# Kernel optimization log

Hardware: AMD Instinct MI355X
Metric: run time of the kernel (lower is better)

Reference implementation:

```python
import jax, jax.numpy as jnp
import numpy as np

B, N, E, DIN, H1, H2, DOUT = 2, 20000, 320000, 128, 256, 256, 128


def setup_inputs() -> dict:
    key = jax.random.key(0)
    ks = jax.random.split(key, 9)
    X = jax.random.normal(ks[0], (B, N, DIN), dtype=jnp.float32)
    edge_index = jax.random.randint(ks[1], (2, E), 0, N, dtype=jnp.int32)
    def lin(k, fan_in, fan_out):
        lim = 1.0 / np.sqrt(fan_in)
        return jax.random.uniform(k, (fan_in, fan_out), jnp.float32, -lim, lim)
    W1 = lin(ks[2], DIN, H1); b1 = jnp.zeros((H1,), jnp.float32)
    W2 = lin(ks[3], H1, H2);  b2 = jnp.zeros((H2,), jnp.float32)
    W3 = lin(ks[4], H2, DOUT); b3 = jnp.zeros((DOUT,), jnp.float32)
    prelu_a = jnp.array(0.25, jnp.float32)  # PReLU default single shared param
    return dict(X=X, W1=W1, b1=b1, W2=W2, b2=b2, W3=W3, b3=b3,
                prelu_a=prelu_a, edge_index=edge_index)


def reference(X, W1, b1, W2, b2, W3, b3, prelu_a, edge_index):
    src, dst = edge_index[0], edge_index[1]
    n = X.shape[1]
    # GCN symmetric normalization with self-loops: deg = in-degree + 1
    deg = jax.ops.segment_sum(jnp.ones_like(src, X.dtype), dst, num_segments=n) + 1.0
    dinv = jax.lax.rsqrt(deg)                      # [N]
    norm_e = dinv[src] * dinv[dst]                 # [E] edge norm
    norm_self = dinv * dinv                        # [N] self-loop norm

    def gcn(x, W, b):
        h = x @ W                                  # [N, F_out]
        agg = jax.ops.segment_sum(h[src] * norm_e[:, None], dst, num_segments=n)
        agg = agg + h * norm_self[:, None]         # add self-loop message
        return agg + b

    def prelu(x):
        return jnp.where(x >= 0, x, prelu_a * x)

    def single(x):  # x: [N, DIN]
        x = prelu(gcn(x, W1, b1))
        x = prelu(gcn(x, W2, b2))
        return gcn(x, W3, b3)

    return jax.vmap(single)(X)                     # [B, N, DOUT]
```

## Files before the change

### kernel.cpp

```cpp
#include <hip/hip_runtime.h>

#define NB 20000
#define EB 320000
#define DIN 128
#define H1D 256
#define H2D 256
#define DOUTD 128
#define SCAN_BLOCKS ((NB + 255) / 256)


__global__ void zero_kernel(int* __restrict__ p, int n) {
    int t = blockIdx.x * blockDim.x + threadIdx.x;
    if (t < n) p[t] = 0;
}

__global__ void hist_kernel(const int* __restrict__ dst, int* __restrict__ bins) {
    int t = blockIdx.x * blockDim.x + threadIdx.x;
    if (t < EB) atomicAdd(&bins[dst[t]], 1);
}

__global__ __launch_bounds__(256) void scanA_kernel(const int* __restrict__ bins,
                                                    int* __restrict__ loc,
                                                    int* __restrict__ blksum) {
    __shared__ int s[256];
    int t = threadIdx.x;
    int i = blockIdx.x * 256 + t;
    int v = (i < NB) ? bins[i] : 0;
    s[t] = v;
    __syncthreads();
    for (int off = 1; off < 256; off <<= 1) {
        int u = (t >= off) ? s[t - off] : 0;
        __syncthreads();
        s[t] += u;
        __syncthreads();
    }
    if (i < NB) loc[i] = s[t] - v;
    if (t == 255) blksum[blockIdx.x] = s[255];
}

__global__ __launch_bounds__(128) void scanB_kernel(int* __restrict__ blksum) {
    __shared__ int s[128];
    int t = threadIdx.x;
    int v = (t < SCAN_BLOCKS) ? blksum[t] : 0;
    s[t] = v;
    __syncthreads();
    for (int off = 1; off < 128; off <<= 1) {
        int u = (t >= off) ? s[t - off] : 0;
        __syncthreads();
        s[t] += u;
        __syncthreads();
    }
    if (t < SCAN_BLOCKS) blksum[t] = s[t] - v;
}

__global__ __launch_bounds__(256) void scanC_kernel(const int* __restrict__ bins,
                                                    const int* __restrict__ loc,
                                                    const int* __restrict__ blksum,
                                                    int* __restrict__ rs,
                                                    int* __restrict__ cursor,
                                                    float* __restrict__ dinv) {
    int i = blockIdx.x * 256 + threadIdx.x;
    if (i < NB) {
        int r = loc[i] + blksum[blockIdx.x];
        rs[i] = r;
        cursor[i] = r;
        dinv[i] = rsqrtf((float)bins[i] + 1.0f);
    }
    if (i == 0) rs[NB] = EB;
}

__global__ void scatter_kernel(const int* __restrict__ src, const int* __restrict__ dst,
                               const float* __restrict__ dinv,
                               int* __restrict__ cursor, int2* __restrict__ edges) {
    int t = blockIdx.x * blockDim.x + threadIdx.x;
    if (t < EB) {
        int d = dst[t], s = src[t];
        int p = atomicAdd(&cursor[d], 1);
        edges[p] = make_int2(s, __float_as_int(dinv[s] * dinv[d]));
    }
}


__device__ inline void vload(float (&d)[4], const float* p) {
    float4 t = *(const float4*)p; d[0] = t.x; d[1] = t.y; d[2] = t.z; d[3] = t.w;
}
__device__ inline void vload(float (&d)[2], const float* p) {
    float2 t = *(const float2*)p; d[0] = t.x; d[1] = t.y;
}
__device__ inline void vstore(float* p, const float (&d)[4]) {
    *(float4*)p = make_float4(d[0], d[1], d[2], d[3]);
}
__device__ inline void vstore(float* p, const float (&d)[2]) {
    *(float2*)p = make_float2(d[0], d[1]);
}

template <int F, bool BIAS, bool PRELU>
__device__ void agg_body(int ablk,
                         const float* __restrict__ h, float* __restrict__ out,
                         const int* __restrict__ rs, const int2* __restrict__ edges,
                         const float* __restrict__ dinv, const float* __restrict__ bias,
                         const float* __restrict__ pa) {
    constexpr int VEC = F / 64;
    int wid = threadIdx.x >> 6;
    int lane = threadIdx.x & 63;
    int node = ablk * 4 + wid;
    const float* hsrc = h + (size_t)lane * VEC;

    float acc0[VEC], acc1[VEC] = {}, acc2[VEC] = {}, acc3[VEC] = {};
    {
        float dv = dinv[node];
        float sw = dv * dv;
        float t[VEC];
        vload(t, hsrc + (size_t)node * F);
#pragma unroll
        for (int v = 0; v < VEC; ++v) acc0[v] = t[v] * sw;
    }
    int e0 = __builtin_amdgcn_readfirstlane(rs[node]);
    int e1 = __builtin_amdgcn_readfirstlane(rs[node + 1]);
    int e = e0;
    for (; e + 4 <= e1; e += 4) {
        int2 d0 = edges[e], d1 = edges[e + 1], d2 = edges[e + 2], d3 = edges[e + 3];
        float t0[VEC], t1[VEC], t2[VEC], t3[VEC];
        vload(t0, hsrc + (size_t)d0.x * F);
        vload(t1, hsrc + (size_t)d1.x * F);
        vload(t2, hsrc + (size_t)d2.x * F);
        vload(t3, hsrc + (size_t)d3.x * F);
        float w0 = __int_as_float(d0.y), w1 = __int_as_float(d1.y);
        float w2 = __int_as_float(d2.y), w3 = __int_as_float(d3.y);
#pragma unroll
        for (int v = 0; v < VEC; ++v) {
            acc0[v] = fmaf(t0[v], w0, acc0[v]);
            acc1[v] = fmaf(t1[v], w1, acc1[v]);
            acc2[v] = fmaf(t2[v], w2, acc2[v]);
            acc3[v] = fmaf(t3[v], w3, acc3[v]);
        }
    }
    for (; e < e1; ++e) {
        int2 d0 = edges[e];
        float t0[VEC];
        vload(t0, hsrc + (size_t)d0.x * F);
        float w0 = __int_as_float(d0.y);
#pragma unroll
        for (int v = 0; v < VEC; ++v) acc0[v] = fmaf(t0[v], w0, acc0[v]);
    }
#pragma unroll
    for (int v = 0; v < VEC; ++v) acc0[v] += (acc1[v] + acc2[v]) + acc3[v];
    if (BIAS) {
        float bv[VEC];
        vload(bv, bias + lane * VEC);
#pragma unroll
        for (int v = 0; v < VEC; ++v) acc0[v] += bv[v];
    }
    if (PRELU) {
        float a = *pa;
#pragma unroll
        for (int v = 0; v < VEC; ++v) acc0[v] = acc0[v] >= 0.0f ? acc0[v] : a * acc0[v];
    }
    vstore(out + (size_t)node * F + lane * VEC, acc0);
}

template <bool BIAS, bool PRELU>
__device__ void gemm_body(int gx, const float* __restrict__ A, int M, int K,
                          const float* __restrict__ W, int Nc,
                          const float* __restrict__ bias, const float* __restrict__ pa,
                          float* __restrict__ C, int mt) {
    __shared__ alignas(16) float As[16][132];
    __shared__ alignas(16) float Bs[16][68];
    int t = threadIdx.x;
    int bm = (gx % mt) * 128;
    int bn = (gx / mt) * 64;
    int tx = t & 15, ty = t >> 4;
    int m0 = ty * 8, n0 = tx * 4;
    int ar = t >> 2, ac4 = (t & 3) * 4;
    int br = t >> 4, bc4 = (t & 15) * 4;

    float acc[8][4] = {};

    for (int k0 = 0; k0 < K; k0 += 16) {
        float4 a0 = make_float4(0.f, 0.f, 0.f, 0.f), a1 = a0;
        int r0 = bm + ar, r1 = bm + ar + 64;
        if (r0 < M) a0 = *(const float4*)&A[(size_t)r0 * K + k0 + ac4];
        if (r1 < M) a1 = *(const float4*)&A[(size_t)r1 * K + k0 + ac4];
        As[ac4 + 0][ar] = a0.x; As[ac4 + 1][ar] = a0.y;
        As[ac4 + 2][ar] = a0.z; As[ac4 + 3][ar] = a0.w;
        As[ac4 + 0][ar + 64] = a1.x; As[ac4 + 1][ar + 64] = a1.y;
        As[ac4 + 2][ar + 64] = a1.z; As[ac4 + 3][ar + 64] = a1.w;
        float4 bv = *(const float4*)&W[(size_t)(k0 + br) * Nc + bn + bc4];
        *(float4*)&Bs[br][bc4] = bv;
        __syncthreads();
#pragma unroll
        for (int k = 0; k < 16; ++k) {
            float4 av0 = *(const float4*)&As[k][m0];
            float4 av1 = *(const float4*)&As[k][m0 + 4];
            float4 bv4 = *(const float4*)&Bs[k][n0];
            float a_[8] = {av0.x, av0.y, av0.z, av0.w, av1.x, av1.y, av1.z, av1.w};
            float b_[4] = {bv4.x, bv4.y, bv4.z, bv4.w};
#pragma unroll
            for (int i = 0; i < 8; ++i)
#pragma unroll
                for (int j = 0; j < 4; ++j)
                    acc[i][j] = fmaf(a_[i], b_[j], acc[i][j]);
        }
        __syncthreads();
    }

    float pav = 0.0f;
    if (PRELU) pav = *pa;
#pragma unroll
    for (int i = 0; i < 8; ++i) {
        int row = bm + m0 + i;
        if (row < M) {
            float v[4];
#pragma unroll
            for (int j = 0; j < 4; ++j) {
                float x = acc[i][j];
                if (BIAS) x += bias[bn + n0 + j];
                if (PRELU) x = (x >= 0.0f) ? x : pav * x;
                v[j] = x;
            }
            *(float4*)&C[(size_t)row * Nc + bn + n0] = make_float4(v[0], v[1], v[2], v[3]);
        }
    }
}


template <int F, bool BIAS, bool PRELU>
__global__ __launch_bounds__(256) void agg_kernel(
    const float* __restrict__ h, float* __restrict__ out,
    const int* __restrict__ rs, const int2* __restrict__ edges,
    const float* __restrict__ dinv, const float* __restrict__ bias,
    const float* __restrict__ pa) {
    agg_body<F, BIAS, PRELU>(blockIdx.x, h, out, rs, edges, dinv, bias, pa);
}

template <bool BIAS, bool PRELU>
__global__ __launch_bounds__(256) void gemm_kernel(
    const float* __restrict__ A, int M, int K, const float* __restrict__ W, int Nc,
    const float* __restrict__ bias, const float* __restrict__ pa,
    float* __restrict__ C, int mt) {
    gemm_body<BIAS, PRELU>(blockIdx.x, A, M, K, W, Nc, bias, pa, C, mt);
}

template <int AF, bool AB, bool AP, bool GB, bool GP>
__global__ __launch_bounds__(256) void fat_kernel(
    const float* __restrict__ A, int M, int K, const float* __restrict__ W, int Nc,
    const float* __restrict__ gbias, float* __restrict__ C, int mt, int ng,
    const float* __restrict__ ah, float* __restrict__ aout,
    const int* __restrict__ rs, const int2* __restrict__ edges,
    const float* __restrict__ dinv, const float* __restrict__ abias,
    const float* __restrict__ pa, int total) {
    int bx = blockIdx.x;
    int p0 = (int)((long long)bx * ng / total);
    int p1 = (int)(((long long)bx + 1) * ng / total);
    if (p1 > p0) {
        gemm_body<GB, GP>(p0, A, M, K, W, Nc, gbias, pa, C, mt);
    } else {
        agg_body<AF, AB, AP>(bx - p1, ah, aout, rs, edges, dinv, abias, pa);
    }
}


static inline char* carve(char*& p, size_t bytes) {
    char* r = p;
    p += (bytes + 255) & ~(size_t)255;
    return r;
}

extern "C" void kernel_launch(void* const* d_in, const int* in_sizes, int n_in,
                              void* d_out, int out_size, void* d_ws, size_t ws_size,
                              hipStream_t stream) {
    const float* X  = (const float*)d_in[0];
    const float* W1 = (const float*)d_in[1];
    const float* b1 = (const float*)d_in[2];
    const float* W2 = (const float*)d_in[3];
    const float* b2 = (const float*)d_in[4];
    const float* W3 = (const float*)d_in[5];
    const float* b3 = (const float*)d_in[6];
    const float* pa = (const float*)d_in[7];
    const int* ei   = (const int*)d_in[8];
    const int* src = ei;
    const int* dst = ei + EB;
    float* out = (float*)d_out;

    char* p = (char*)d_ws;
    int* bins    = (int*)carve(p, NB * sizeof(int));
    int* loc     = (int*)carve(p, NB * sizeof(int));
    int* blksum  = (int*)carve(p, 128 * sizeof(int));
    int* rs      = (int*)carve(p, (NB + 1) * sizeof(int));
    int* cursor  = (int*)carve(p, NB * sizeof(int));
    int2* edges  = (int2*)carve(p, EB * sizeof(int2));
    float* dinv  = (float*)carve(p, NB * sizeof(float));
    float* P0 = (float*)carve(p, (size_t)NB * 256 * sizeof(float));
    float* Q0 = (float*)carve(p, (size_t)NB * 256 * sizeof(float));
    float* P1 = (float*)carve(p, (size_t)NB * 256 * sizeof(float));
    float* Q1 = (float*)carve(p, (size_t)NB * 256 * sizeof(float));

    const float* X0 = X;
    const float* X1 = X + (size_t)NB * DIN;
    float* out0 = out;
    float* out1 = out + (size_t)NB * DOUTD;

    zero_kernel<<<SCAN_BLOCKS, 256, 0, stream>>>(bins, NB);
    hist_kernel<<<(EB + 255) / 256, 256, 0, stream>>>(dst, bins);
    scanA_kernel<<<SCAN_BLOCKS, 256, 0, stream>>>(bins, loc, blksum);
    scanB_kernel<<<1, 128, 0, stream>>>(blksum);
    scanC_kernel<<<SCAN_BLOCKS, 256, 0, stream>>>(bins, loc, blksum, rs, cursor, dinv);
    scatter_kernel<<<(EB + 255) / 256, 256, 0, stream>>>(src, dst, dinv, cursor, edges);

    const int AGG_BLK = NB / 4;
    const int MT = (NB + 127) / 128;
    const int NG_256 = MT * (256 / 64);
    const int NG_128 = MT * (128 / 64);


    agg_kernel<128, false, false><<<AGG_BLK, 256, 0, stream>>>(
        X0, P0, rs, edges, dinv, nullptr, nullptr);

    fat_kernel<128, false, false, true, true><<<NG_256 + AGG_BLK, 256, 0, stream>>>(
        P0, NB, DIN, W1, H1D, b1, Q0, MT, NG_256,
        X1, P1, rs, edges, dinv, nullptr, pa, NG_256 + AGG_BLK);

    gemm_kernel<false, false><<<NG_256, 256, 0, stream>>>(
        Q0, NB, H1D, W2, H2D, nullptr, nullptr, P0, MT);
    gemm_kernel<true, true><<<NG_256, 256, 0, stream>>>(
        P1, NB, DIN, W1, H1D, b1, pa, Q1, MT);

    fat_kernel<256, true, true, false, false><<<NG_256 + AGG_BLK, 256, 0, stream>>>(
        Q1, NB, H1D, W2, H2D, nullptr, P1, MT, NG_256,
        P0, Q0, rs, edges, dinv, b2, pa, NG_256 + AGG_BLK);

    fat_kernel<256, true, true, false, false><<<NG_128 + AGG_BLK, 256, 0, stream>>>(
        Q0, NB, H2D, W3, DOUTD, nullptr, P0, MT, NG_128,
        P1, Q1, rs, edges, dinv, b2, pa, NG_128 + AGG_BLK);

    fat_kernel<128, true, false, false, false><<<NG_128 + AGG_BLK, 256, 0, stream>>>(
        Q1, NB, H2D, W3, DOUTD, nullptr, P1, MT, NG_128,
        P0, out0, rs, edges, dinv, b3, nullptr, NG_128 + AGG_BLK);

    agg_kernel<128, true, false><<<AGG_BLK, 256, 0, stream>>>(
        P1, out1, rs, edges, dinv, b3, nullptr);
}
```

Before: 444.9 us.

## Slice aggregation by feature columns per XCD, enlarge GEMM tile, add nontemporal accesses

After: 1.081 ms. 2.43x slower.

```diff
diff --git a/kernel.cpp b/kernel.cpp
--- a/kernel.cpp
+++ b/kernel.cpp
@@ -7,6 +7,17 @@
 #define H2D 256
 #define DOUTD 128
 #define SCAN_BLOCKS ((NB + 255) / 256)
+
+typedef __attribute__((ext_vector_type(4))) float fvec4;
+
+__device__ inline float4 ntload4(const float* p) {
+    fvec4 v = __builtin_nontemporal_load((const fvec4*)p);
+    return make_float4(v.x, v.y, v.z, v.w);
+}
+__device__ inline void ntstore4(float* p, float4 v) {
+    fvec4 t; t.x = v.x; t.y = v.y; t.z = v.z; t.w = v.w;
+    __builtin_nontemporal_store(t, (fvec4*)p);
+}
 
 
 __global__ void zero_kernel(int* __restrict__ p, int n) {
@@ -81,82 +92,87 @@
 }
 
 
-__device__ inline void vload(float (&d)[4], const float* p) {
-    float4 t = *(const float4*)p; d[0] = t.x; d[1] = t.y; d[2] = t.z; d[3] = t.w;
-}
-__device__ inline void vload(float (&d)[2], const float* p) {
-    float2 t = *(const float2*)p; d[0] = t.x; d[1] = t.y;
-}
-__device__ inline void vstore(float* p, const float (&d)[4]) {
-    *(float4*)p = make_float4(d[0], d[1], d[2], d[3]);
-}
-__device__ inline void vstore(float* p, const float (&d)[2]) {
-    *(float2*)p = make_float2(d[0], d[1]);
-}
-
-template <int F, bool BIAS, bool PRELU>
-__device__ void agg_body(int ablk,
-                         const float* __restrict__ h, float* __restrict__ out,
-                         const int* __restrict__ rs, const int2* __restrict__ edges,
-                         const float* __restrict__ dinv, const float* __restrict__ bias,
-                         const float* __restrict__ pa) {
-    constexpr int VEC = F / 64;
-    int wid = threadIdx.x >> 6;
-    int lane = threadIdx.x & 63;
-    int node = ablk * 4 + wid;
-    const float* hsrc = h + (size_t)lane * VEC;
-
-    float acc0[VEC], acc1[VEC] = {}, acc2[VEC] = {}, acc3[VEC] = {};
-    {
-        float dv = dinv[node];
-        float sw = dv * dv;
-        float t[VEC];
-        vload(t, hsrc + (size_t)node * F);
-#pragma unroll
-        for (int v = 0; v < VEC; ++v) acc0[v] = t[v] * sw;
-    }
-    int e0 = __builtin_amdgcn_readfirstlane(rs[node]);
-    int e1 = __builtin_amdgcn_readfirstlane(rs[node + 1]);
-    int e = e0;
-    for (; e + 4 <= e1; e += 4) {
-        int2 d0 = edges[e], d1 = edges[e + 1], d2 = edges[e + 2], d3 = edges[e + 3];
-        float t0[VEC], t1[VEC], t2[VEC], t3[VEC];
-        vload(t0, hsrc + (size_t)d0.x * F);
-        vload(t1, hsrc + (size_t)d1.x * F);
-        vload(t2, hsrc + (size_t)d2.x * F);
-        vload(t3, hsrc + (size_t)d3.x * F);
-        float w0 = __int_as_float(d0.y), w1 = __int_as_float(d1.y);
-        float w2 = __int_as_float(d2.y), w3 = __int_as_float(d3.y);
-#pragma unroll
-        for (int v = 0; v < VEC; ++v) {
-            acc0[v] = fmaf(t0[v], w0, acc0[v]);
-            acc1[v] = fmaf(t1[v], w1, acc1[v]);
-            acc2[v] = fmaf(t2[v], w2, acc2[v]);
-            acc3[v] = fmaf(t3[v], w3, acc3[v]);
-        }
-    }
-    for (; e < e1; ++e) {
-        int2 d0 = edges[e];
-        float t0[VEC];
-        vload(t0, hsrc + (size_t)d0.x * F);
-        float w0 = __int_as_float(d0.y);
-#pragma unroll
-        for (int v = 0; v < VEC; ++v) acc0[v] = fmaf(t0[v], w0, acc0[v]);
-    }
-#pragma unroll
-    for (int v = 0; v < VEC; ++v) acc0[v] += (acc1[v] + acc2[v]) + acc3[v];
-    if (BIAS) {
-        float bv[VEC];
-        vload(bv, bias + lane * VEC);
-#pragma unroll
-        for (int v = 0; v < VEC; ++v) acc0[v] += bv[v];
-    }
-    if (PRELU) {
-        float a = *pa;
-#pragma unroll
-        for (int v = 0; v < VEC; ++v) acc0[v] = acc0[v] >= 0.0f ? acc0[v] : a * acc0[v];
-    }
-    vstore(out + (size_t)node * F + lane * VEC, acc0);
+template <int F, bool BIAS, bool PRELU, bool NTE>
+__device__ void aggs_body(int a, int xcd,
+                          const float* __restrict__ h, float* __restrict__ out,
+                          const int* __restrict__ rs, const int2* __restrict__ edges,
+                          const float* __restrict__ dinv, const float* __restrict__ bias,
+                          const float* __restrict__ pa) {
+    constexpr int NS = F / 32;
+    constexpr int NH = 8 / NS;
+    constexpr int CG = (F == 128) ? 125 : 250;
+    constexpr int NPB = NB / NH / CG;
+    constexpr int NPW = NPB / 4;
+
+    const int s32 = xcd & (NS - 1);
+    const int half = xcd / NS;
+    const int chunk = a >> 3;
+    const int wid = threadIdx.x >> 6;
+    const int lane = threadIdx.x & 63;
+    const int li = lane & 31;
+    const int eh = lane >> 5;
+
+    const float* gb = h + s32 * 32 + li;
+    const float pav = PRELU ? *pa : 0.0f;
+    const float bval = BIAS ? bias[s32 * 32 + li] : 0.0f;
+
+    int n = half * (NB / NH) + chunk * NPB + wid * NPW;
+    int e1 = __builtin_amdgcn_readfirstlane(rs[n]);
+    for (int j = 0; j < NPW; ++j, ++n) {
+        int e0 = e1;
+        e1 = __builtin_amdgcn_readfirstlane(rs[n + 1]);
+        float a0 = 0.f, a1 = 0.f, a2 = 0.f, a3 = 0.f;
+        int e = e0;
+        for (; e + 8 <= e1; e += 8) {
+            int s0, s1, s2, s3;
+            float w0, w1, w2, w3;
+            if (NTE) {
+                long long r0 = __builtin_nontemporal_load((const long long*)(edges + e + eh));
+                long long r1 = __builtin_nontemporal_load((const long long*)(edges + e + 2 + eh));
+                long long r2 = __builtin_nontemporal_load((const long long*)(edges + e + 4 + eh));
+                long long r3 = __builtin_nontemporal_load((const long long*)(edges + e + 6 + eh));
+                s0 = (int)r0; w0 = __int_as_float((int)(r0 >> 32));
+                s1 = (int)r1; w1 = __int_as_float((int)(r1 >> 32));
+                s2 = (int)r2; w2 = __int_as_float((int)(r2 >> 32));
+                s3 = (int)r3; w3 = __int_as_float((int)(r3 >> 32));
+            } else {
+                int2 r0 = edges[e + eh], r1 = edges[e + 2 + eh];
+                int2 r2 = edges[e + 4 + eh], r3 = edges[e + 6 + eh];
+                s0 = r0.x; w0 = __int_as_float(r0.y);
+                s1 = r1.x; w1 = __int_as_float(r1.y);
+                s2 = r2.x; w2 = __int_as_float(r2.y);
+                s3 = r3.x; w3 = __int_as_float(r3.y);
+            }
+            float t0 = gb[(size_t)s0 * F];
+            float t1 = gb[(size_t)s1 * F];
+            float t2 = gb[(size_t)s2 * F];
+            float t3 = gb[(size_t)s3 * F];
+            a0 = fmaf(t0, w0, a0);
+            a1 = fmaf(t1, w1, a1);
+            a2 = fmaf(t2, w2, a2);
+            a3 = fmaf(t3, w3, a3);
+        }
+        for (; e + 2 <= e1; e += 2) {
+            int2 r0 = edges[e + eh];
+            a0 = fmaf(gb[(size_t)r0.x * F], __int_as_float(r0.y), a0);
+        }
+        if (e < e1) {
+            int my = e + eh;
+            bool valid = (my < e1);
+            int2 r0 = edges[valid ? my : e];
+            float w = valid ? __int_as_float(r0.y) : 0.0f;
+            a0 = fmaf(gb[(size_t)r0.x * F], w, a0);
+        }
+        float acc = (a0 + a1) + (a2 + a3);
+        acc += __shfl_xor(acc, 32, 64);
+        float dv = dinv[n];
+        float ts = gb[(size_t)n * F];
+        float r = fmaf(ts, dv * dv, acc);
+        if (BIAS) r += bval;
+        if (PRELU) r = (r >= 0.0f) ? r : pav * r;
+        if (eh == 0)
+            __builtin_nontemporal_store(r, out + (size_t)n * F + s32 * 32 + li);
+    }
 }
 
 template <bool BIAS, bool PRELU>
@@ -165,38 +181,43 @@
                           const float* __restrict__ bias, const float* __restrict__ pa,
                           float* __restrict__ C, int mt) {
     __shared__ alignas(16) float As[16][132];
-    __shared__ alignas(16) float Bs[16][68];
+    __shared__ alignas(16) float Bs[16][132];
     int t = threadIdx.x;
     int bm = (gx % mt) * 128;
-    int bn = (gx / mt) * 64;
-    int tx = t & 15, ty = t >> 4;
-    int m0 = ty * 8, n0 = tx * 4;
+    int bn = (gx / mt) * 128;
+    int tx = t & 31, ty = t >> 5;
+    int m0 = ty * 16, n0 = tx * 4;
     int ar = t >> 2, ac4 = (t & 3) * 4;
-    int br = t >> 4, bc4 = (t & 15) * 4;
-
-    float acc[8][4] = {};
+    int bk = t >> 4, bc4 = (t & 15) * 4;
+
+    float acc[16][4] = {};
 
     for (int k0 = 0; k0 < K; k0 += 16) {
         float4 a0 = make_float4(0.f, 0.f, 0.f, 0.f), a1 = a0;
         int r0 = bm + ar, r1 = bm + ar + 64;
-        if (r0 < M) a0 = *(const float4*)&A[(size_t)r0 * K + k0 + ac4];
-        if (r1 < M) a1 = *(const float4*)&A[(size_t)r1 * K + k0 + ac4];
+        if (r0 < M) a0 = ntload4(&A[(size_t)r0 * K + k0 + ac4]);
+        if (r1 < M) a1 = ntload4(&A[(size_t)r1 * K + k0 + ac4]);
         As[ac4 + 0][ar] = a0.x; As[ac4 + 1][ar] = a0.y;
         As[ac4 + 2][ar] = a0.z; As[ac4 + 3][ar] = a0.w;
         As[ac4 + 0][ar + 64] = a1.x; As[ac4 + 1][ar + 64] = a1.y;
         As[ac4 + 2][ar + 64] = a1.z; As[ac4 + 3][ar + 64] = a1.w;
-        float4 bv = *(const float4*)&W[(size_t)(k0 + br) * Nc + bn + bc4];
-        *(float4*)&Bs[br][bc4] = bv;
+        float4 b0 = *(const float4*)&W[(size_t)(k0 + bk) * Nc + bn + bc4];
+        float4 b1 = *(const float4*)&W[(size_t)(k0 + bk) * Nc + bn + bc4 + 64];
+        *(float4*)&Bs[bk][bc4] = b0;
+        *(float4*)&Bs[bk][bc4 + 64] = b1;
         __syncthreads();
 #pragma unroll
         for (int k = 0; k < 16; ++k) {
             float4 av0 = *(const float4*)&As[k][m0];
             float4 av1 = *(const float4*)&As[k][m0 + 4];
-            float4 bv4 = *(const float4*)&Bs[k][n0];
-            float a_[8] = {av0.x, av0.y, av0.z, av0.w, av1.x, av1.y, av1.z, av1.w};
-            float b_[4] = {bv4.x, bv4.y, bv4.z, bv4.w};
-#pragma unroll
-            for (int i = 0; i < 8; ++i)
+            float4 av2 = *(const float4*)&As[k][m0 + 8];
+            float4 av3 = *(const float4*)&As[k][m0 + 12];
+            float4 bv = *(const float4*)&Bs[k][n0];
+            float a_[16] = {av0.x, av0.y, av0.z, av0.w, av1.x, av1.y, av1.z, av1.w,
+                            av2.x, av2.y, av2.z, av2.w, av3.x, av3.y, av3.z, av3.w};
+            float b_[4] = {bv.x, bv.y, bv.z, bv.w};
+#pragma unroll
+            for (int i = 0; i < 16; ++i)
 #pragma unroll
                 for (int j = 0; j < 4; ++j)
                     acc[i][j] = fmaf(a_[i], b_[j], acc[i][j]);
@@ -207,7 +228,7 @@
     float pav = 0.0f;
     if (PRELU) pav = *pa;
 #pragma unroll
-    for (int i = 0; i < 8; ++i) {
+    for (int i = 0; i < 16; ++i) {
         int row = bm + m0 + i;
         if (row < M) {
             float v[4];
@@ -218,19 +239,20 @@
                 if (PRELU) x = (x >= 0.0f) ? x : pav * x;
                 v[j] = x;
             }
-            *(float4*)&C[(size_t)row * Nc + bn + n0] = make_float4(v[0], v[1], v[2], v[3]);
-        }
-    }
-}
-
-
-template <int F, bool BIAS, bool PRELU>
+            ntstore4(&C[(size_t)row * Nc + bn + n0], make_float4(v[0], v[1], v[2], v[3]));
+        }
+    }
+}
+
+
+template <int F, bool BIAS, bool PRELU, bool NTE>
 __global__ __launch_bounds__(256) void agg_kernel(
     const float* __restrict__ h, float* __restrict__ out,
     const int* __restrict__ rs, const int2* __restrict__ edges,
     const float* __restrict__ dinv, const float* __restrict__ bias,
     const float* __restrict__ pa) {
-    agg_body<F, BIAS, PRELU>(blockIdx.x, h, out, rs, edges, dinv, bias, pa);
+    aggs_body<F, BIAS, PRELU, NTE>(blockIdx.x, blockIdx.x & 7, h, out, rs, edges,
+                                   dinv, bias, pa);
 }
 
 template <bool BIAS, bool PRELU>
@@ -241,21 +263,20 @@
     gemm_body<BIAS, PRELU>(blockIdx.x, A, M, K, W, Nc, bias, pa, C, mt);
 }
 
-template <int AF, bool AB, bool AP, bool GB, bool GP>
+template <int AF, bool AB, bool AP, bool ANTE, bool GB_, bool GP>
 __global__ __launch_bounds__(256) void fat_kernel(
-    const float* __restrict__ A, int M, int K, const float* __restrict__ W, int Nc,
+    const float* __restrict__ A, int K, const float* __restrict__ W, int Nc,
     const float* __restrict__ gbias, float* __restrict__ C, int mt, int ng,
     const float* __restrict__ ah, float* __restrict__ aout,
     const int* __restrict__ rs, const int2* __restrict__ edges,
     const float* __restrict__ dinv, const float* __restrict__ abias,
-    const float* __restrict__ pa, int total) {
+    const float* __restrict__ pa) {
     int bx = blockIdx.x;
-    int p0 = (int)((long long)bx * ng / total);
-    int p1 = (int)(((long long)bx + 1) * ng / total);
-    if (p1 > p0) {
-        gemm_body<GB, GP>(p0, A, M, K, W, Nc, gbias, pa, C, mt);
+    if (bx < ng) {
+        gemm_body<GB_, GP>(bx, A, NB, K, W, Nc, gbias, pa, C, mt);
     } else {
-        agg_body<AF, AB, AP>(bx - p1, ah, aout, rs, edges, dinv, abias, pa);
+        aggs_body<AF, AB, AP, ANTE>(bx - ng, bx & 7, ah, aout, rs, edges, dinv,
+                                    abias, pa);
     }
 }
 
@@ -307,36 +328,37 @@
     scanC_kernel<<<SCAN_BLOCKS, 256, 0, stream>>>(bins, loc, blksum, rs, cursor, dinv);
     scatter_kernel<<<(EB + 255) / 256, 256, 0, stream>>>(src, dst, dinv, cursor, edges);
 
-    const int AGG_BLK = NB / 4;
     const int MT = (NB + 127) / 128;
-    const int NG_256 = MT * (256 / 64);
-    const int NG_128 = MT * (128 / 64);
-
-
-    agg_kernel<128, false, false><<<AGG_BLK, 256, 0, stream>>>(
+    const int NG_256 = MT * (256 / 128);
+    const int NG_128 = MT * (128 / 128);
+    const int AGG128 = 8 * 125;
+    const int AGG256 = 8 * 250;
+
+
+    agg_kernel<128, false, false, false><<<AGG128, 256, 0, stream>>>(
         X0, P0, rs, edges, dinv, nullptr, nullptr);
 
-    fat_kernel<128, false, false, true, true><<<NG_256 + AGG_BLK, 256, 0, stream>>>(
-        P0, NB, DIN, W1, H1D, b1, Q0, MT, NG_256,
-        X1, P1, rs, edges, dinv, nullptr, pa, NG_256 + AGG_BLK);
+    fat_kernel<128, false, false, false, true, true><<<NG_256 + AGG128, 256, 0, stream>>>(
+        P0, DIN, W1, H1D, b1, Q0, MT, NG_256,
+        X1, P1, rs, edges, dinv, nullptr, pa);
 
     gemm_kernel<false, false><<<NG_256, 256, 0, stream>>>(
-        Q0, NB, H1D, W2, H2D, nullptr, nullptr, P0, MT);
+        Q0, NB, H1D, W2, H2D, nullptr, pa, P0, MT);
     gemm_kernel<true, true><<<NG_256, 256, 0, stream>>>(
         P1, NB, DIN, W1, H1D, b1, pa, Q1, MT);
 
-    fat_kernel<256, true, true, false, false><<<NG_256 + AGG_BLK, 256, 0, stream>>>(
-        Q1, NB, H1D, W2, H2D, nullptr, P1, MT, NG_256,
-        P0, Q0, rs, edges, dinv, b2, pa, NG_256 + AGG_BLK);
-
-    fat_kernel<256, true, true, false, false><<<NG_128 + AGG_BLK, 256, 0, stream>>>(
-        Q0, NB, H2D, W3, DOUTD, nullptr, P0, MT, NG_128,
-        P1, Q1, rs, edges, dinv, b2, pa, NG_128 + AGG_BLK);
-
-    fat_kernel<128, true, false, false, false><<<NG_128 + AGG_BLK, 256, 0, stream>>>(
-        Q1, NB, H2D, W3, DOUTD, nullptr, P1, MT, NG_128,
-        P0, out0, rs, edges, dinv, b3, nullptr, NG_128 + AGG_BLK);
-
-    agg_kernel<128, true, false><<<AGG_BLK, 256, 0, stream>>>(
+    fat_kernel<256, true, true, true, false, false><<<NG_256 + AGG256, 256, 0, stream>>>(
+        Q1, H1D, W2, H2D, nullptr, P1, MT, NG_256,
+        P0, Q0, rs, edges, dinv, b2, pa);
+
+    fat_kernel<256, true, true, true, false, false><<<NG_128 + AGG256, 256, 0, stream>>>(
+        Q0, H2D, W3, DOUTD, nullptr, P0, MT, NG_128,
+        P1, Q1, rs, edges, dinv, b2, pa);
+
+    fat_kernel<128, true, false, false, false, false><<<NG_128 + AGG128, 256, 0, stream>>>(
+        Q1, H2D, W3, DOUTD, nullptr, P1, MT, NG_128,
+        P0, out0, rs, edges, dinv, b3, pa);
+
+    agg_kernel<128, true, false, false><<<AGG128, 256, 0, stream>>>(
         P1, out1, rs, edges, dinv, b3, nullptr);
 }
```
